# Kernel optimization log

Hardware: AMD Instinct MI355X
Metric: run time of the kernel (lower is better)

## Reference

```python
import jax, jax.numpy as jnp
import numpy as np

B = 32
H_TEX, W_TEX, C = 512, 512, 3
N = H_TEX * W_TEX * C          # flattened texture length per sample
OH, OW = 128, 64               # bbox_size
M = OH * OW * C                # rows of each per-sample sparse matrix
NNZ = 98304                    # nonzeros per sample (4 per output element)


def setup_inputs() -> dict:
    key = jax.random.key(0)
    k1, k2, k3, k4 = jax.random.split(key, 4)
    x = jax.random.normal(k1, (B, C, H_TEX, W_TEX), dtype=jnp.float32)
    rows = jax.random.randint(k2, (B, NNZ), 0, M, dtype=jnp.int32)
    cols = jax.random.randint(k3, (B, NNZ), 0, N, dtype=jnp.int32)
    vals = jax.random.uniform(k4, (B, NNZ), dtype=jnp.float32)
    mask = jnp.ones((B, C, OH, OW), dtype=jnp.float32)
    return {"x": x, "rows": rows, "cols": cols, "vals": vals, "mask": mask}


def reference(x, rows, cols, vals, mask):
    # x: (B, C, H, W) -> channels-last flat per sample, matching x.permute(0,2,3,1).reshape(B,-1)
    xf = jnp.transpose(x, (0, 2, 3, 1)).reshape(B, -1)          # (B, N)
    # Batched sparse mm: out[b, m] = sum_{k: rows[b,k]==m} vals[b,k] * xf[b, cols[b,k]]
    gathered = vals * jnp.take_along_axis(xf, cols, axis=1)     # (B, NNZ)
    seg_ids = (rows.astype(jnp.int32) + jnp.arange(B, dtype=jnp.int32)[:, None] * M).reshape(-1)
    out_flat = jax.ops.segment_sum(gathered.reshape(-1), seg_ids, num_segments=B * M)
    result = out_flat.reshape(B, OH, OW, C).transpose(0, 3, 1, 2)  # (B, C, 128, 64)
    return result, mask
```

## Files before the change

### kernel.cpp

```cpp
#include <hip/hip_runtime.h>

#define BATCH 32
#define CCH 3
#define HW_TEX (512 * 512)
#define N_TEX (HW_TEX * CCH)
#define OH 128
#define OW 64
#define P_OUT (OH * OW)
#define M_OUT (P_OUT * CCH)
#define NNZ 98304
#define OUT_ELEMS (BATCH * M_OUT)

#define BLOCK 1024

#define WS_SEG8 ((size_t)32 * 8 * M_OUT * 4)
#define WS_SEG4 ((size_t)32 * 4 * M_OUT * 4)

template <int NSEG>
__global__ __launch_bounds__(BLOCK) void scan_full_kernel(
    const float* __restrict__ x,
    const int*   __restrict__ rows,
    const int*   __restrict__ cols,
    const float* __restrict__ vals,
    float* __restrict__ partial) {
    __shared__ __align__(16) float acc[M_OUT];

    const int blk = blockIdx.x;
    const int s   = blk & 31;
    const int seg = blk >> 5;
    const int t   = threadIdx.x;

    float4* acc4 = reinterpret_cast<float4*>(acc);
#pragma unroll
    for (int j = 0; j < M_OUT / 4 / BLOCK; ++j)
        acc4[t + j * BLOCK] = make_float4(0.f, 0.f, 0.f, 0.f);
    __syncthreads();

    constexpr int SEGN = NNZ / NSEG;
    const size_t  off  = (size_t)s * NNZ + (size_t)seg * SEGN;
    const int4*   r4 = reinterpret_cast<const int4*>(rows + off);
    const int4*   c4 = reinterpret_cast<const int4*>(cols + off);
    const float4* v4 = reinterpret_cast<const float4*>(vals + off);
    const float*  xs = x + (size_t)s * N_TEX;

#pragma unroll
    for (int j = 0; j < SEGN / (BLOCK * 4); ++j) {
        int4   r = r4[j * BLOCK + t];
        int4   c = c4[j * BLOCK + t];
        float4 v = v4[j * BLOCK + t];

        float g0 = xs[(c.x % CCH) * HW_TEX + c.x / CCH];
        float g1 = xs[(c.y % CCH) * HW_TEX + c.y / CCH];
        float g2 = xs[(c.z % CCH) * HW_TEX + c.z / CCH];
        float g3 = xs[(c.w % CCH) * HW_TEX + c.w / CCH];

        atomicAdd(&acc[r.x], v.x * g0);
        atomicAdd(&acc[r.y], v.y * g1);
        atomicAdd(&acc[r.z], v.z * g2);
        atomicAdd(&acc[r.w], v.w * g3);
    }
    __syncthreads();

    float4* pp = reinterpret_cast<float4*>(partial + (size_t)blk * M_OUT);
#pragma unroll
    for (int j = 0; j < M_OUT / 4 / BLOCK; ++j)
        pp[t + j * BLOCK] = acc4[t + j * BLOCK];
}

__global__ __launch_bounds__(256) void reduce_kernel(
    const float* __restrict__ partial,
    const float* __restrict__ mask,
    float* __restrict__ out, int nseg) {
    int tid = blockIdx.x * 256 + threadIdx.x;
    if (tid >= OUT_ELEMS) return;
    int s   = tid / M_OUT;
    int rcl = tid % M_OUT;
    float sum = 0.f;
    for (int seg = 0; seg < nseg; ++seg)
        sum += partial[(size_t)(seg * 32 + s) * M_OUT + rcl];
    int ch = rcl % CCH;
    int p  = rcl / CCH;
    out[(size_t)s * M_OUT + ch * P_OUT + p] = sum;
    out[OUT_ELEMS + tid] = mask[tid];
}

#define CHUNKS 8
#define RPC (M_OUT / CHUNKS)
__global__ __launch_bounds__(BLOCK) void spmm_chunk_kernel(
    const float* __restrict__ x,
    const int*   __restrict__ rows,
    const int*   __restrict__ cols,
    const float* __restrict__ vals,
    const float* __restrict__ mask,
    float* __restrict__ out) {
    __shared__ float acc[RPC];
    const int blk = blockIdx.x;
    const int s   = blk / CHUNKS;
    const int c   = blk % CHUNKS;
    const int t   = threadIdx.x;
    const int rbase = c * RPC;
#pragma unroll
    for (int j = 0; j < RPC / BLOCK; ++j) acc[t + j * BLOCK] = 0.0f;
    __syncthreads();
    const int*   rs = rows + (size_t)s * NNZ;
    const int*   cs = cols + (size_t)s * NNZ;
    const float* vs = vals + (size_t)s * NNZ;
    const float* xs = x    + (size_t)s * N_TEX;
#pragma unroll 4
    for (int i = t; i < NNZ; i += BLOCK) {
        int r = rs[i];
        unsigned lr = (unsigned)(r - rbase);
        if (lr < (unsigned)RPC) {
            int   col = cs[i];
            float v   = vs[i];
            atomicAdd(&acc[lr], v * xs[(col % CCH) * HW_TEX + col / CCH]);
        }
    }
    __syncthreads();
    const size_t outbase = (size_t)s * M_OUT;
#pragma unroll
    for (int ch = 0; ch < CCH; ++ch)
        out[outbase + (size_t)ch * P_OUT + c * (P_OUT / CHUNKS) + t] = acc[t * CCH + ch];
    {
        float* mout = out + OUT_ELEMS;
        const int base = blk * RPC;
#pragma unroll
        for (int j = 0; j < RPC / BLOCK; ++j)
            mout[base + j * BLOCK + t] = mask[base + j * BLOCK + t];
    }
}

extern "C" void kernel_launch(void* const* d_in, const int* in_sizes, int n_in,
                              void* d_out, int out_size, void* d_ws, size_t ws_size,
                              hipStream_t stream) {
    const float* x    = (const float*)d_in[0];
    const int*   rows = (const int*)  d_in[1];
    const int*   cols = (const int*)  d_in[2];
    const float* vals = (const float*)d_in[3];
    const float* mask = (const float*)d_in[4];
    float* out = (float*)d_out;

    if (ws_size >= WS_SEG8) {
        float* partial = (float*)d_ws;
        scan_full_kernel<8><<<32 * 8, BLOCK, 0, stream>>>(x, rows, cols, vals, partial);
        reduce_kernel<<<(OUT_ELEMS + 255) / 256, 256, 0, stream>>>(partial, mask, out, 8);
    } else if (ws_size >= WS_SEG4) {
        float* partial = (float*)d_ws;
        scan_full_kernel<4><<<32 * 4, BLOCK, 0, stream>>>(x, rows, cols, vals, partial);
        reduce_kernel<<<(OUT_ELEMS + 255) / 256, 256, 0, stream>>>(partial, mask, out, 4);
    } else {
        spmm_chunk_kernel<<<BATCH * CHUNKS, BLOCK, 0, stream>>>(x, rows, cols, vals, mask, out);
    }
}
```

Measured before the change: 208.5 us.

## Split each sample into 32 segments with XCD-aware block mapping and vectorize reduce

Adds a scan kernel that splits each sample's nonzeros into 32 segments of 3072, one 768-thread block each, for 1024 blocks in total. Block indices are mapped so that all segments of a sample stay on one XCD, which helps L2 reuse of that sample's texture. The reduce kernel now reads and sums float4 partials and copies the mask with float4 accesses. In exchange the workspace needs are larger and the reduce reads 32 partial buffers instead of 8, plus each block spends more time zeroing and writing back its full 96 KB shared accumulator relative to the little work it does.

```diff
diff --git a/kernel.cpp b/kernel.cpp
--- a/kernel.cpp
+++ b/kernel.cpp
@@ -11,11 +11,55 @@
 #define NNZ 98304
 #define OUT_ELEMS (BATCH * M_OUT)
 
+#define WS32 ((size_t)32 * 32 * M_OUT * 4)
+#define WS8  ((size_t)32 * 8  * M_OUT * 4)
+
+#define B32 768
+__global__ __launch_bounds__(B32) void scan32_kernel(
+    const float* __restrict__ x,
+    const int*   __restrict__ rows,
+    const int*   __restrict__ cols,
+    const float* __restrict__ vals,
+    float* __restrict__ partial) {
+    __shared__ __align__(16) float acc[M_OUT];
+
+    const int blk = blockIdx.x;
+    const int xcd = blk & 7;
+    const int seg = (blk >> 3) & 31;
+    const int rnd = blk >> 8;
+    const int s   = rnd * 8 + xcd;
+    const int t   = threadIdx.x;
+
+    float4* acc4 = reinterpret_cast<float4*>(acc);
+#pragma unroll
+    for (int j = 0; j < M_OUT / 4 / B32; ++j)
+        acc4[t + j * B32] = make_float4(0.f, 0.f, 0.f, 0.f);
+    __syncthreads();
+
+    const size_t off = (size_t)s * NNZ + (size_t)seg * (NNZ / 32);
+    int4   r = reinterpret_cast<const int4*>(rows + off)[t];
+    int4   c = reinterpret_cast<const int4*>(cols + off)[t];
+    float4 v = reinterpret_cast<const float4*>(vals + off)[t];
+    const float* xs = x + (size_t)s * N_TEX;
+
+    float g0 = xs[(c.x % CCH) * HW_TEX + c.x / CCH];
+    float g1 = xs[(c.y % CCH) * HW_TEX + c.y / CCH];
+    float g2 = xs[(c.z % CCH) * HW_TEX + c.z / CCH];
+    float g3 = xs[(c.w % CCH) * HW_TEX + c.w / CCH];
+
+    atomicAdd(&acc[r.x], v.x * g0);
+    atomicAdd(&acc[r.y], v.y * g1);
+    atomicAdd(&acc[r.z], v.z * g2);
+    atomicAdd(&acc[r.w], v.w * g3);
+    __syncthreads();
+
+    float4* pp = reinterpret_cast<float4*>(partial + (size_t)(seg * 32 + s) * M_OUT);
+#pragma unroll
+    for (int j = 0; j < M_OUT / 4 / B32; ++j)
+        pp[t + j * B32] = acc4[t + j * B32];
+}
+
 #define BLOCK 1024
-
-#define WS_SEG8 ((size_t)32 * 8 * M_OUT * 4)
-#define WS_SEG4 ((size_t)32 * 4 * M_OUT * 4)
-
 template <int NSEG>
 __global__ __launch_bounds__(BLOCK) void scan_full_kernel(
     const float* __restrict__ x,
@@ -24,44 +68,37 @@
     const float* __restrict__ vals,
     float* __restrict__ partial) {
     __shared__ __align__(16) float acc[M_OUT];
-
     const int blk = blockIdx.x;
     const int s   = blk & 31;
     const int seg = blk >> 5;
     const int t   = threadIdx.x;
-
     float4* acc4 = reinterpret_cast<float4*>(acc);
 #pragma unroll
     for (int j = 0; j < M_OUT / 4 / BLOCK; ++j)
         acc4[t + j * BLOCK] = make_float4(0.f, 0.f, 0.f, 0.f);
     __syncthreads();
-
     constexpr int SEGN = NNZ / NSEG;
     const size_t  off  = (size_t)s * NNZ + (size_t)seg * SEGN;
     const int4*   r4 = reinterpret_cast<const int4*>(rows + off);
     const int4*   c4 = reinterpret_cast<const int4*>(cols + off);
     const float4* v4 = reinterpret_cast<const float4*>(vals + off);
     const float*  xs = x + (size_t)s * N_TEX;
-
 #pragma unroll
     for (int j = 0; j < SEGN / (BLOCK * 4); ++j) {
         int4   r = r4[j * BLOCK + t];
         int4   c = c4[j * BLOCK + t];
         float4 v = v4[j * BLOCK + t];
-
         float g0 = xs[(c.x % CCH) * HW_TEX + c.x / CCH];
         float g1 = xs[(c.y % CCH) * HW_TEX + c.y / CCH];
         float g2 = xs[(c.z % CCH) * HW_TEX + c.z / CCH];
         float g3 = xs[(c.w % CCH) * HW_TEX + c.w / CCH];
-
         atomicAdd(&acc[r.x], v.x * g0);
         atomicAdd(&acc[r.y], v.y * g1);
         atomicAdd(&acc[r.z], v.z * g2);
         atomicAdd(&acc[r.w], v.w * g3);
     }
     __syncthreads();
-
-    float4* pp = reinterpret_cast<float4*>(partial + (size_t)blk * M_OUT);
+    float4* pp = reinterpret_cast<float4*>(partial + (size_t)(seg * 32 + s) * M_OUT);
 #pragma unroll
     for (int j = 0; j < M_OUT / 4 / BLOCK; ++j)
         pp[t + j * BLOCK] = acc4[t + j * BLOCK];
@@ -72,16 +109,25 @@
     const float* __restrict__ mask,
     float* __restrict__ out, int nseg) {
     int tid = blockIdx.x * 256 + threadIdx.x;
-    if (tid >= OUT_ELEMS) return;
-    int s   = tid / M_OUT;
-    int rcl = tid % M_OUT;
-    float sum = 0.f;
-    for (int seg = 0; seg < nseg; ++seg)
-        sum += partial[(size_t)(seg * 32 + s) * M_OUT + rcl];
-    int ch = rcl % CCH;
-    int p  = rcl / CCH;
-    out[(size_t)s * M_OUT + ch * P_OUT + p] = sum;
-    out[OUT_ELEMS + tid] = mask[tid];
+    if (tid >= OUT_ELEMS / 4) return;
+    int s    = tid / (M_OUT / 4);
+    int rcl4 = (tid % (M_OUT / 4)) * 4;
+
+    const float4* pp = reinterpret_cast<const float4*>(
+        partial + (size_t)s * M_OUT + rcl4);
+    const size_t stride4 = (size_t)32 * M_OUT / 4;
+    float4 sum = make_float4(0.f, 0.f, 0.f, 0.f);
+    for (int seg = 0; seg < nseg; ++seg) {
+        float4 p = pp[(size_t)seg * stride4];
+        sum.x += p.x; sum.y += p.y; sum.z += p.z; sum.w += p.w;
+    }
+    float* ob = out + (size_t)s * M_OUT;
+    ob[(rcl4 + 0) % CCH * P_OUT + (rcl4 + 0) / CCH] = sum.x;
+    ob[(rcl4 + 1) % CCH * P_OUT + (rcl4 + 1) / CCH] = sum.y;
+    ob[(rcl4 + 2) % CCH * P_OUT + (rcl4 + 2) / CCH] = sum.z;
+    ob[(rcl4 + 3) % CCH * P_OUT + (rcl4 + 3) / CCH] = sum.w;
+    reinterpret_cast<float4*>(out + OUT_ELEMS)[tid] =
+        reinterpret_cast<const float4*>(mask)[tid];
 }
 
 #define CHUNKS 8
@@ -139,15 +185,16 @@
     const float* vals = (const float*)d_in[3];
     const float* mask = (const float*)d_in[4];
     float* out = (float*)d_out;
-
-    if (ws_size >= WS_SEG8) {
+    int rgrid = (OUT_ELEMS / 4 + 255) / 256;
+
+    if (ws_size >= WS32) {
+        float* partial = (float*)d_ws;
+        scan32_kernel<<<1024, B32, 0, stream>>>(x, rows, cols, vals, partial);
+        reduce_kernel<<<rgrid, 256, 0, stream>>>(partial, mask, out, 32);
+    } else if (ws_size >= WS8) {
         float* partial = (float*)d_ws;
         scan_full_kernel<8><<<32 * 8, BLOCK, 0, stream>>>(x, rows, cols, vals, partial);
-        reduce_kernel<<<(OUT_ELEMS + 255) / 256, 256, 0, stream>>>(partial, mask, out, 8);
-    } else if (ws_size >= WS_SEG4) {
-        float* partial = (float*)d_ws;
-        scan_full_kernel<4><<<32 * 4, BLOCK, 0, stream>>>(x, rows, cols, vals, partial);
-        reduce_kernel<<<(OUT_ELEMS + 255) / 256, 256, 0, stream>>>(partial, mask, out, 4);
+        reduce_kernel<<<rgrid, 256, 0, stream>>>(partial, mask, out, 8);
     } else {
         spmm_chunk_kernel<<<BATCH * CHUNKS, BLOCK, 0, stream>>>(x, rows, cols, vals, mask, out);
     }
```

New measurement: 226.1 us. +8.4%, slower.

## Split scan into row chunks with XCD-aware sample mapping and vectorized reduce

Applied to the files above, without the earlier changes.

The scan kernel now gives each block a quarter of the output rows in shared memory (24 KB instead of 96 KB) and one eighth of the nonzeros. Each block loops over four samples, and samples are mapped to blocks by XCD index so that one sample's texture stays within one XCD's L2. Because blocks skip nonzeros outside their row chunk, each nonzero is read by four blocks and only gathers on a hit. The smaller LDS footprint is meant to allow more resident blocks and better L2 locality for the random gathers, at the cost of reading the index streams four times. The reduce kernel now handles four elements per thread with float4 loads.

```diff
diff --git a/kernel.cpp b/kernel.cpp
--- a/kernel.cpp
+++ b/kernel.cpp
@@ -11,81 +11,111 @@
 #define NNZ 98304
 #define OUT_ELEMS (BATCH * M_OUT)
 
-#define BLOCK 1024
+#define NCH 4
+#define RPCH (M_OUT / NCH)
+#define NE 8
+#define SEGE (NNZ / NE)
+#define TB 1024
+#define NROUND 4
 
-#define WS_SEG8 ((size_t)32 * 8 * M_OUT * 4)
-#define WS_SEG4 ((size_t)32 * 4 * M_OUT * 4)
+#define WS_NEED ((size_t)BATCH * NCH * NE * RPCH * 4)
+#define WS8     ((size_t)32 * 8 * M_OUT * 4)
 
-template <int NSEG>
-__global__ __launch_bounds__(BLOCK) void scan_full_kernel(
+__global__ __launch_bounds__(TB) void scan_chunk_kernel(
     const float* __restrict__ x,
     const int*   __restrict__ rows,
     const int*   __restrict__ cols,
     const float* __restrict__ vals,
     float* __restrict__ partial) {
-    __shared__ __align__(16) float acc[M_OUT];
+    __shared__ __align__(16) float acc[RPCH];
 
-    const int blk = blockIdx.x;
-    const int s   = blk & 31;
-    const int seg = blk >> 5;
-    const int t   = threadIdx.x;
+    const int blk  = blockIdx.x;
+    const int xcd  = blk & 7;
+    const int slot = blk >> 3;
+    const int c    = slot & (NCH - 1);
+    const int e    = slot >> 2;
+    const int t    = threadIdx.x;
+    const int rbase = c * RPCH;
 
-    float4* acc4 = reinterpret_cast<float4*>(acc);
+    for (int rnd = 0; rnd < NROUND; ++rnd) {
+        const int s = rnd * 8 + xcd;
+
+        float2* acc2 = reinterpret_cast<float2*>(acc);
 #pragma unroll
-    for (int j = 0; j < M_OUT / 4 / BLOCK; ++j)
-        acc4[t + j * BLOCK] = make_float4(0.f, 0.f, 0.f, 0.f);
-    __syncthreads();
+        for (int j = 0; j < RPCH / 2 / TB; ++j)
+            acc2[t + j * TB] = make_float2(0.f, 0.f);
+        __syncthreads();
 
-    constexpr int SEGN = NNZ / NSEG;
-    const size_t  off  = (size_t)s * NNZ + (size_t)seg * SEGN;
-    const int4*   r4 = reinterpret_cast<const int4*>(rows + off);
-    const int4*   c4 = reinterpret_cast<const int4*>(cols + off);
-    const float4* v4 = reinterpret_cast<const float4*>(vals + off);
-    const float*  xs = x + (size_t)s * N_TEX;
+        const size_t off = (size_t)s * NNZ + (size_t)e * SEGE;
+        const int4*   r4 = reinterpret_cast<const int4*>(rows + off);
+        const int4*   c4 = reinterpret_cast<const int4*>(cols + off);
+        const float4* v4 = reinterpret_cast<const float4*>(vals + off);
+        const float*  xs = x + (size_t)s * N_TEX;
+
+        int4 r[3], cc[3]; float4 v[3];
+#pragma unroll
+        for (int j = 0; j < 3; ++j) {
+            r[j]  = r4[j * TB + t];
+            cc[j] = c4[j * TB + t];
+            v[j]  = v4[j * TB + t];
+        }
 
 #pragma unroll
-    for (int j = 0; j < SEGN / (BLOCK * 4); ++j) {
-        int4   r = r4[j * BLOCK + t];
-        int4   c = c4[j * BLOCK + t];
-        float4 v = v4[j * BLOCK + t];
+        for (int j = 0; j < 3; ++j) {
+            int  ri[4] = {r[j].x, r[j].y, r[j].z, r[j].w};
+            int  ci[4] = {cc[j].x, cc[j].y, cc[j].z, cc[j].w};
+            float vi[4] = {v[j].x, v[j].y, v[j].z, v[j].w};
+#pragma unroll
+            for (int k = 0; k < 4; ++k) {
+                unsigned lr = (unsigned)(ri[k] - rbase);
+                bool in = lr < (unsigned)RPCH;
+                int gi = in ? ((ci[k] % CCH) * HW_TEX + ci[k] / CCH) : 0;
+                float g = xs[gi];
+                if (in) atomicAdd(&acc[lr], vi[k] * g);
+            }
+        }
+        __syncthreads();
 
-        float g0 = xs[(c.x % CCH) * HW_TEX + c.x / CCH];
-        float g1 = xs[(c.y % CCH) * HW_TEX + c.y / CCH];
-        float g2 = xs[(c.z % CCH) * HW_TEX + c.z / CCH];
-        float g3 = xs[(c.w % CCH) * HW_TEX + c.w / CCH];
-
-        atomicAdd(&acc[r.x], v.x * g0);
-        atomicAdd(&acc[r.y], v.y * g1);
-        atomicAdd(&acc[r.z], v.z * g2);
-        atomicAdd(&acc[r.w], v.w * g3);
+        float2* pp = reinterpret_cast<float2*>(
+            partial + (((size_t)s * NCH + c) * NE + e) * RPCH);
+#pragma unroll
+        for (int j = 0; j < RPCH / 2 / TB; ++j)
+            pp[t + j * TB] = acc2[t + j * TB];
+        __syncthreads();
     }
-    __syncthreads();
-
-    float4* pp = reinterpret_cast<float4*>(partial + (size_t)blk * M_OUT);
-#pragma unroll
-    for (int j = 0; j < M_OUT / 4 / BLOCK; ++j)
-        pp[t + j * BLOCK] = acc4[t + j * BLOCK];
 }
 
-__global__ __launch_bounds__(256) void reduce_kernel(
+__global__ __launch_bounds__(256) void reduce_chunk_kernel(
     const float* __restrict__ partial,
     const float* __restrict__ mask,
-    float* __restrict__ out, int nseg) {
+    float* __restrict__ out) {
     int tid = blockIdx.x * 256 + threadIdx.x;
-    if (tid >= OUT_ELEMS) return;
-    int s   = tid / M_OUT;
-    int rcl = tid % M_OUT;
-    float sum = 0.f;
-    for (int seg = 0; seg < nseg; ++seg)
-        sum += partial[(size_t)(seg * 32 + s) * M_OUT + rcl];
-    int ch = rcl % CCH;
-    int p  = rcl / CCH;
-    out[(size_t)s * M_OUT + ch * P_OUT + p] = sum;
-    out[OUT_ELEMS + tid] = mask[tid];
+    if (tid >= OUT_ELEMS / 4) return;
+    int s    = tid / (M_OUT / 4);
+    int rcl4 = (tid % (M_OUT / 4)) * 4;
+    int c    = rcl4 / RPCH;
+    int lr4  = rcl4 % RPCH;
+
+    const float4* pp = reinterpret_cast<const float4*>(
+        partial + (((size_t)s * NCH + c) * NE) * RPCH + lr4);
+    float4 sum = make_float4(0.f, 0.f, 0.f, 0.f);
+#pragma unroll
+    for (int e = 0; e < NE; ++e) {
+        float4 p = pp[(size_t)e * (RPCH / 4)];
+        sum.x += p.x; sum.y += p.y; sum.z += p.z; sum.w += p.w;
+    }
+    float* ob = out + (size_t)s * M_OUT;
+    ob[(rcl4 + 0) % CCH * P_OUT + (rcl4 + 0) / CCH] = sum.x;
+    ob[(rcl4 + 1) % CCH * P_OUT + (rcl4 + 1) / CCH] = sum.y;
+    ob[(rcl4 + 2) % CCH * P_OUT + (rcl4 + 2) / CCH] = sum.z;
+    ob[(rcl4 + 3) % CCH * P_OUT + (rcl4 + 3) / CCH] = sum.w;
+    reinterpret_cast<float4*>(out + OUT_ELEMS)[tid] =
+        reinterpret_cast<const float4*>(mask)[tid];
 }
 
 #define CHUNKS 8
 #define RPC (M_OUT / CHUNKS)
+#define BLOCK 1024
 __global__ __launch_bounds__(BLOCK) void spmm_chunk_kernel(
     const float* __restrict__ x,
     const int*   __restrict__ rows,
@@ -139,15 +169,12 @@
     const float* vals = (const float*)d_in[3];
     const float* mask = (const float*)d_in[4];
     float* out = (float*)d_out;
+    int rgrid = (OUT_ELEMS / 4 + 255) / 256;
 
-    if (ws_size >= WS_SEG8) {
+    if (ws_size >= WS_NEED) {
         float* partial = (float*)d_ws;
-        scan_full_kernel<8><<<32 * 8, BLOCK, 0, stream>>>(x, rows, cols, vals, partial);
-        reduce_kernel<<<(OUT_ELEMS + 255) / 256, 256, 0, stream>>>(partial, mask, out, 8);
-    } else if (ws_size >= WS_SEG4) {
-        float* partial = (float*)d_ws;
-        scan_full_kernel<4><<<32 * 4, BLOCK, 0, stream>>>(x, rows, cols, vals, partial);
-        reduce_kernel<<<(OUT_ELEMS + 255) / 256, 256, 0, stream>>>(partial, mask, out, 4);
+        scan_chunk_kernel<<<256, TB, 0, stream>>>(x, rows, cols, vals, partial);
+        reduce_chunk_kernel<<<rgrid, 256, 0, stream>>>(partial, mask, out);
     } else {
         spmm_chunk_kernel<<<BATCH * CHUNKS, BLOCK, 0, stream>>>(x, rows, cols, vals, mask, out);
     }
```

Measured after the change: 206.3 us. No clear change (-1.1%).

## Split gather from LDS scatter into separate kernels and vectorize reduce

Applied to the files above, without the earlier changes.

Splits the fused gather+atomic kernel into a high-occupancy gather kernel (1536 blocks of 256) that writes vals*x to a workspace buffer, then a scatter kernel with 4 segments per sample doing shared-memory atomics. The random texture gathers get far more parallelism to hide latency, where before they ran only in the large LDS-bound blocks. The reduce now reads float4 across 4 partials, and the mask copy moves into the gather kernel. This adds a kernel launch and an extra round trip of the gathered values through global memory.

```diff
diff --git a/kernel.cpp b/kernel.cpp
--- a/kernel.cpp
+++ b/kernel.cpp
@@ -11,81 +11,110 @@
 #define NNZ 98304
 #define OUT_ELEMS (BATCH * M_OUT)
 
-#define BLOCK 1024
+#define NQ 4
+#define WS_NEED ((size_t)BATCH * NNZ * 4 + (size_t)BATCH * NQ * M_OUT * 4)
 
-#define WS_SEG8 ((size_t)32 * 8 * M_OUT * 4)
-#define WS_SEG4 ((size_t)32 * 4 * M_OUT * 4)
-
-template <int NSEG>
-__global__ __launch_bounds__(BLOCK) void scan_full_kernel(
+__global__ __launch_bounds__(256) void gather_kernel(
     const float* __restrict__ x,
-    const int*   __restrict__ rows,
     const int*   __restrict__ cols,
     const float* __restrict__ vals,
+    float* __restrict__ g,
+    const float* __restrict__ mask,
+    float* __restrict__ out) {
+    const int blk = blockIdx.x;
+    const int s   = blk / 48;
+    const int t   = threadIdx.x;
+    const size_t off = (size_t)s * NNZ + (size_t)(blk % 48) * 2048;
+
+    const int4*   c4 = reinterpret_cast<const int4*>(cols + off);
+    const float4* v4 = reinterpret_cast<const float4*>(vals + off);
+    float4*       g4 = reinterpret_cast<float4*>(g + off);
+    const float*  xs = x + (size_t)s * N_TEX;
+
+    int4   ca = c4[t],       cb = c4[t + 256];
+    float4 va = v4[t],       vb = v4[t + 256];
+
+    float4 ga, gb;
+    ga.x = va.x * xs[(ca.x % CCH) * HW_TEX + ca.x / CCH];
+    ga.y = va.y * xs[(ca.y % CCH) * HW_TEX + ca.y / CCH];
+    ga.z = va.z * xs[(ca.z % CCH) * HW_TEX + ca.z / CCH];
+    ga.w = va.w * xs[(ca.w % CCH) * HW_TEX + ca.w / CCH];
+    gb.x = vb.x * xs[(cb.x % CCH) * HW_TEX + cb.x / CCH];
+    gb.y = vb.y * xs[(cb.y % CCH) * HW_TEX + cb.y / CCH];
+    gb.z = vb.z * xs[(cb.z % CCH) * HW_TEX + cb.z / CCH];
+    gb.w = vb.w * xs[(cb.w % CCH) * HW_TEX + cb.w / CCH];
+
+    g4[t]       = ga;
+    g4[t + 256] = gb;
+
+    reinterpret_cast<float2*>(out + OUT_ELEMS)[blk * 256 + t] =
+        reinterpret_cast<const float2*>(mask)[blk * 256 + t];
+}
+
+__global__ __launch_bounds__(1024) void scatter_kernel(
+    const int*   __restrict__ rows,
+    const float* __restrict__ g,
     float* __restrict__ partial) {
     __shared__ __align__(16) float acc[M_OUT];
 
     const int blk = blockIdx.x;
-    const int s   = blk & 31;
-    const int seg = blk >> 5;
+    const int s   = blk >> 2;
+    const int q   = blk & 3;
     const int t   = threadIdx.x;
 
     float4* acc4 = reinterpret_cast<float4*>(acc);
 #pragma unroll
-    for (int j = 0; j < M_OUT / 4 / BLOCK; ++j)
-        acc4[t + j * BLOCK] = make_float4(0.f, 0.f, 0.f, 0.f);
+    for (int j = 0; j < M_OUT / 4 / 1024; ++j)
+        acc4[t + j * 1024] = make_float4(0.f, 0.f, 0.f, 0.f);
     __syncthreads();
 
-    constexpr int SEGN = NNZ / NSEG;
-    const size_t  off  = (size_t)s * NNZ + (size_t)seg * SEGN;
+    const size_t off = (size_t)s * NNZ + (size_t)q * (NNZ / NQ);
     const int4*   r4 = reinterpret_cast<const int4*>(rows + off);
-    const int4*   c4 = reinterpret_cast<const int4*>(cols + off);
-    const float4* v4 = reinterpret_cast<const float4*>(vals + off);
-    const float*  xs = x + (size_t)s * N_TEX;
+    const float4* g4 = reinterpret_cast<const float4*>(g + off);
 
 #pragma unroll
-    for (int j = 0; j < SEGN / (BLOCK * 4); ++j) {
-        int4   r = r4[j * BLOCK + t];
-        int4   c = c4[j * BLOCK + t];
-        float4 v = v4[j * BLOCK + t];
-
-        float g0 = xs[(c.x % CCH) * HW_TEX + c.x / CCH];
-        float g1 = xs[(c.y % CCH) * HW_TEX + c.y / CCH];
-        float g2 = xs[(c.z % CCH) * HW_TEX + c.z / CCH];
-        float g3 = xs[(c.w % CCH) * HW_TEX + c.w / CCH];
-
-        atomicAdd(&acc[r.x], v.x * g0);
-        atomicAdd(&acc[r.y], v.y * g1);
-        atomicAdd(&acc[r.z], v.z * g2);
-        atomicAdd(&acc[r.w], v.w * g3);
+    for (int j = 0; j < 6; ++j) {
+        int4   r = r4[j * 1024 + t];
+        float4 v = g4[j * 1024 + t];
+        atomicAdd(&acc[r.x], v.x);
+        atomicAdd(&acc[r.y], v.y);
+        atomicAdd(&acc[r.z], v.z);
+        atomicAdd(&acc[r.w], v.w);
     }
     __syncthreads();
 
     float4* pp = reinterpret_cast<float4*>(partial + (size_t)blk * M_OUT);
 #pragma unroll
-    for (int j = 0; j < M_OUT / 4 / BLOCK; ++j)
-        pp[t + j * BLOCK] = acc4[t + j * BLOCK];
+    for (int j = 0; j < M_OUT / 4 / 1024; ++j)
+        pp[t + j * 1024] = acc4[t + j * 1024];
 }
 
 __global__ __launch_bounds__(256) void reduce_kernel(
     const float* __restrict__ partial,
-    const float* __restrict__ mask,
-    float* __restrict__ out, int nseg) {
+    float* __restrict__ out) {
     int tid = blockIdx.x * 256 + threadIdx.x;
-    if (tid >= OUT_ELEMS) return;
-    int s   = tid / M_OUT;
-    int rcl = tid % M_OUT;
-    float sum = 0.f;
-    for (int seg = 0; seg < nseg; ++seg)
-        sum += partial[(size_t)(seg * 32 + s) * M_OUT + rcl];
-    int ch = rcl % CCH;
-    int p  = rcl / CCH;
-    out[(size_t)s * M_OUT + ch * P_OUT + p] = sum;
-    out[OUT_ELEMS + tid] = mask[tid];
+    if (tid >= OUT_ELEMS / 4) return;
+    int s    = tid / (M_OUT / 4);
+    int rcl4 = (tid % (M_OUT / 4)) * 4;
+
+    const float4* pp = reinterpret_cast<const float4*>(
+        partial + (size_t)(s * NQ) * M_OUT + rcl4);
+    float4 sum = make_float4(0.f, 0.f, 0.f, 0.f);
+#pragma unroll
+    for (int q = 0; q < NQ; ++q) {
+        float4 p = pp[(size_t)q * (M_OUT / 4)];
+        sum.x += p.x; sum.y += p.y; sum.z += p.z; sum.w += p.w;
+    }
+    float* ob = out + (size_t)s * M_OUT;
+    ob[(rcl4 + 0) % CCH * P_OUT + (rcl4 + 0) / CCH] = sum.x;
+    ob[(rcl4 + 1) % CCH * P_OUT + (rcl4 + 1) / CCH] = sum.y;
+    ob[(rcl4 + 2) % CCH * P_OUT + (rcl4 + 2) / CCH] = sum.z;
+    ob[(rcl4 + 3) % CCH * P_OUT + (rcl4 + 3) / CCH] = sum.w;
 }
 
 #define CHUNKS 8
 #define RPC (M_OUT / CHUNKS)
+#define BLOCK 1024
 __global__ __launch_bounds__(BLOCK) void spmm_chunk_kernel(
     const float* __restrict__ x,
     const int*   __restrict__ rows,
@@ -140,14 +169,12 @@
     const float* mask = (const float*)d_in[4];
     float* out = (float*)d_out;
 
-    if (ws_size >= WS_SEG8) {
-        float* partial = (float*)d_ws;
-        scan_full_kernel<8><<<32 * 8, BLOCK, 0, stream>>>(x, rows, cols, vals, partial);
-        reduce_kernel<<<(OUT_ELEMS + 255) / 256, 256, 0, stream>>>(partial, mask, out, 8);
-    } else if (ws_size >= WS_SEG4) {
-        float* partial = (float*)d_ws;
-        scan_full_kernel<4><<<32 * 4, BLOCK, 0, stream>>>(x, rows, cols, vals, partial);
-        reduce_kernel<<<(OUT_ELEMS + 255) / 256, 256, 0, stream>>>(partial, mask, out, 4);
+    if (ws_size >= WS_NEED) {
+        float* g       = (float*)d_ws;
+        float* partial = g + (size_t)BATCH * NNZ;
+        gather_kernel<<<1536, 256, 0, stream>>>(x, cols, vals, g, mask, out);
+        scatter_kernel<<<BATCH * NQ, 1024, 0, stream>>>(rows, g, partial);
+        reduce_kernel<<<(OUT_ELEMS / 4 + 255) / 256, 256, 0, stream>>>(partial, out);
     } else {
         spmm_chunk_kernel<<<BATCH * CHUNKS, BLOCK, 0, stream>>>(x, rows, cols, vals, mask, out);
     }
```

After: 231.8 us. 11.1% more time.
